# Optimization experiments

Measured on AMD Instinct MI355X. Metric: run time of the kernel, lower is better.

## Reference

```python
import jax, jax.numpy as jnp
import numpy as np

ADAPTERS = 40   # adapter_num, hard-coded by range(40) and tsv 40x40
CAPS = 3        # num_capsules
CLASS_DIM = 200 # MAX_SEQ
IN_CH = CAPS * CLASS_DIM  # 600
B = 256
D = 768
NUM_ITERS = 3


def squash(v, axis=-1):
    sq = jnp.sum(v * v, axis=axis, keepdims=True)
    return (sq / (1.0 + sq)) * v / jnp.sqrt(sq)


def setup_inputs() -> dict:
    key = jax.random.key(0)
    k0, k1, k2, k3, k4 = jax.random.split(key, 5)
    x = jax.random.normal(k0, (B, ADAPTERS, IN_CH), jnp.float32)
    s = jax.random.uniform(k1, (1,), jnp.float32) * 4.0 + 1.0  # gate temperature
    route_weights = jax.random.normal(k2, (ADAPTERS, CAPS, IN_CH, CLASS_DIM), jnp.float32)
    larger_w = jax.random.normal(k3, (D, CAPS), jnp.float32) * 0.1  # Linear(3,768) weight [out,in]
    larger_b = jnp.zeros((D,), jnp.float32)
    elarger = jax.random.normal(k4, (ADAPTERS, D), jnp.float32)     # Embedding(40,768)
    tsv = jnp.tril(jnp.ones((ADAPTERS, ADAPTERS), jnp.float32))
    return {"t": 20, "x": x, "s": s, "route_weights": route_weights,
            "larger_w": larger_w, "larger_b": larger_b, "elarger": elarger, "tsv": tsv}


def reference(t, x, s, route_weights, larger_w, larger_b, elarger, tsv):
    bz = x.shape[0]
    # per-adapter small matmuls, batched: priors[n,b,k,d] = sum_c x[b,k,c] * W[k,n,c,d]
    priors = jnp.einsum('bkc,kncd->nbkd', x, route_weights)[:, :, :, None, :]  # [3,B,40,1,200]
    tsv_t = tsv[t]                                   # [40]
    mask = jnp.where(tsv_t == 0, -10000.0, 0.0)      # [40]
    tsv_b = tsv_t[None, None, :, None, None]
    mask_b = mask[None, None, :, None, None]
    logits = jnp.zeros_like(priors)
    vote = None
    for i in range(NUM_ITERS):
        logits = logits * tsv_b + mask_b
        probs = jax.nn.softmax(logits, axis=2)       # my_softmax over adapter dim
        vote = jnp.sum(probs * priors, axis=2, keepdims=True)   # [3,B,1,1,200]
        out = squash(vote, axis=-1)
        if i != NUM_ITERS - 1:
            logits = logits + jnp.sum(priors * out, axis=-1, keepdims=True)
    # torch's .view(bz, length, -1) on a [3,B,1,1,200] tensor: row-major reinterpretation
    h = vote.reshape(bz, CLASS_DIM, CAPS)            # [B,200,3]
    h = h @ larger_w.T + larger_b                    # [B,200,768]
    g = jax.nn.sigmoid(s * elarger[t])               # [768] (broadcast of [1]*[768])
    return h * g
```

## Files before the change

kernel.cpp:

```cpp
#include <hip/hip_runtime.h>
#include <hip/hip_bf16.h>

#define ADAPTERS 40
#define CAPS 3
#define IN_CH 600
#define BSZ 256
#define DCLS 200
#define DMODEL 768

typedef __attribute__((ext_vector_type(8))) short short8;
typedef __attribute__((ext_vector_type(4))) float f32x4;
typedef __attribute__((ext_vector_type(4))) float f4v;

__global__ void k0_gw(const float* __restrict__ s_p,
                      const float* __restrict__ lw,
                      const float* __restrict__ lb,
                      const float* __restrict__ el,
                      const int* __restrict__ t_p,
                      float4* __restrict__ gw4) {
    int j = blockIdx.x * blockDim.x + threadIdx.x;
    if (j >= DMODEL) return;
    float s = s_p[0];
    int t = t_p[0];
    float e = el[t * DMODEL + j];
    float g = 1.0f / (1.0f + expf(-s * e));
    gw4[j] = make_float4(g * lw[j * 3 + 0], g * lw[j * 3 + 1],
                         g * lw[j * 3 + 2], g * lb[j]);
}

#define RP 40
#define NCHUNK 19

__device__ __forceinline__ void split2(float f0, float f1,
                                       unsigned& hi, unsigned& lo) {
    unsigned u0 = __float_as_uint(f0), u1 = __float_as_uint(f1);
    unsigned h0 = u0 & 0xFFFF0000u, h1 = u1 & 0xFFFF0000u;
    hi = (u0 >> 16) | h1;
    float l0 = f0 - __uint_as_float(h0);
    float l1 = f1 - __uint_as_float(h1);
    lo = (__float_as_uint(l0) >> 16) | (__float_as_uint(l1) & 0xFFFF0000u);
}

__global__ __launch_bounds__(256) void k1_priors(
    const float* __restrict__ x,
    const float* __restrict__ rw,
    const float* __restrict__ tsv,
    const int* __restrict__ t_p,
    float* __restrict__ priors)
{
    int kk = blockIdx.z;
    int t = t_p[0];
    if (tsv[t * ADAPTERS + kk] == 0.0f) return;

    int b0 = blockIdx.x * 128;
    int j0 = blockIdx.y * 128;

    __shared__ __align__(16) unsigned short Ahi[128 * RP];
    __shared__ __align__(16) unsigned short Alo[128 * RP];
    __shared__ __align__(16) unsigned short Bhi[128 * RP];
    __shared__ __align__(16) unsigned short Blo[128 * RP];

    int tid = threadIdx.x;
    int lane = tid & 63, w = tid >> 6;
    int lm = lane & 15, lq = lane >> 4;
    int m0w = (w & 1) * 64, n0w = (w >> 1) * 64;

    int a_bi = tid >> 1;
    int a_ci0 = (tid & 1) * 16;
    const float* a_row = x + ((size_t)(b0 + a_bi) * ADAPTERS + kk) * IN_CH;
    int b_jj = tid >> 1;
    int b_ci0 = (tid & 1) * 16;
    int j = j0 + b_jj;
    bool jvalid = (j < CAPS * DCLS);
    int cap = (j >= 2 * DCLS) ? 2 : ((j >= DCLS) ? 1 : 0);
    int d = j - cap * DCLS;
    const float* b_base = rw + ((size_t)(kk * 3 + cap) * IN_CH) * DCLS + d;

    f32x4 acc[4][4];
    #pragma unroll
    for (int mt = 0; mt < 4; mt++)
        #pragma unroll
        for (int nt = 0; nt < 4; nt++)
            acc[mt][nt] = (f32x4){0.f, 0.f, 0.f, 0.f};

    float4 ax[4];
    float  bx[16];

    {
        int c0 = 0;
        #pragma unroll
        for (int q = 0; q < 4; q++) {
            int c = c0 + a_ci0 + q * 4;
            ax[q] = (c + 4 <= IN_CH) ? *(const float4*)(a_row + c)
                                     : make_float4(0.f, 0.f, 0.f, 0.f);
        }
        #pragma unroll
        for (int i = 0; i < 16; i++) {
            int c = c0 + b_ci0 + i;
            bx[i] = (jvalid && c < IN_CH) ? b_base[(size_t)c * DCLS] : 0.f;
        }
    }

    for (int ch = 0; ch < NCHUNK; ch++) {
        unsigned ahi[8], alo[8], bhi[8], blo[8];
        #pragma unroll
        for (int q = 0; q < 4; q++) {
            split2(ax[q].x, ax[q].y, ahi[q * 2], alo[q * 2]);
            split2(ax[q].z, ax[q].w, ahi[q * 2 + 1], alo[q * 2 + 1]);
        }
        #pragma unroll
        for (int p = 0; p < 8; p++)
            split2(bx[2 * p], bx[2 * p + 1], bhi[p], blo[p]);

        __syncthreads();
        {
            unsigned* pa = (unsigned*)&Ahi[a_bi * RP + a_ci0];
            *(uint4*)pa = make_uint4(ahi[0], ahi[1], ahi[2], ahi[3]);
            *(uint4*)(pa + 4) = make_uint4(ahi[4], ahi[5], ahi[6], ahi[7]);
            unsigned* pl = (unsigned*)&Alo[a_bi * RP + a_ci0];
            *(uint4*)pl = make_uint4(alo[0], alo[1], alo[2], alo[3]);
            *(uint4*)(pl + 4) = make_uint4(alo[4], alo[5], alo[6], alo[7]);
            unsigned* pb = (unsigned*)&Bhi[b_jj * RP + b_ci0];
            *(uint4*)pb = make_uint4(bhi[0], bhi[1], bhi[2], bhi[3]);
            *(uint4*)(pb + 4) = make_uint4(bhi[4], bhi[5], bhi[6], bhi[7]);
            unsigned* pc = (unsigned*)&Blo[b_jj * RP + b_ci0];
            *(uint4*)pc = make_uint4(blo[0], blo[1], blo[2], blo[3]);
            *(uint4*)(pc + 4) = make_uint4(blo[4], blo[5], blo[6], blo[7]);
        }
        __syncthreads();

        if (ch + 1 < NCHUNK) {
            int c0 = (ch + 1) * 32;
            #pragma unroll
            for (int q = 0; q < 4; q++) {
                int c = c0 + a_ci0 + q * 4;
                ax[q] = (c + 4 <= IN_CH) ? *(const float4*)(a_row + c)
                                         : make_float4(0.f, 0.f, 0.f, 0.f);
            }
            #pragma unroll
            for (int i = 0; i < 16; i++) {
                int c = c0 + b_ci0 + i;
                bx[i] = (jvalid && c < IN_CH) ? b_base[(size_t)c * DCLS] : 0.f;
            }
        }

        short8 Afh[4], Afl[4];
        #pragma unroll
        for (int mt = 0; mt < 4; mt++) {
            int row = m0w + mt * 16 + lm;
            Afh[mt] = *(const short8*)&Ahi[row * RP + lq * 8];
            Afl[mt] = *(const short8*)&Alo[row * RP + lq * 8];
        }
        #pragma unroll
        for (int nt = 0; nt < 4; nt++) {
            int row = n0w + nt * 16 + lm;
            short8 bh = *(const short8*)&Bhi[row * RP + lq * 8];
            short8 bl = *(const short8*)&Blo[row * RP + lq * 8];
            #pragma unroll
            for (int mt = 0; mt < 4; mt++) {
                acc[mt][nt] = __builtin_amdgcn_mfma_f32_16x16x32_bf16(
                    bh, Afh[mt], acc[mt][nt], 0, 0, 0);
                acc[mt][nt] = __builtin_amdgcn_mfma_f32_16x16x32_bf16(
                    bl, Afh[mt], acc[mt][nt], 0, 0, 0);
                acc[mt][nt] = __builtin_amdgcn_mfma_f32_16x16x32_bf16(
                    bh, Afl[mt], acc[mt][nt], 0, 0, 0);
            }
        }
    }

    #pragma unroll
    for (int nt = 0; nt < 4; nt++) {
        int jc = j0 + n0w + nt * 16 + lq * 4;
        if (jc >= CAPS * DCLS) continue;
        int capc = (jc >= 2 * DCLS) ? 2 : ((jc >= DCLS) ? 1 : 0);
        int dc = jc - capc * DCLS;
        #pragma unroll
        for (int mt = 0; mt < 4; mt++) {
            int b = b0 + m0w + mt * 16 + lm;
            float* dst = priors +
                ((size_t)(capc * BSZ + b) * ADAPTERS + kk) * DCLS + dc;
            *(f4v*)dst = *(f4v*)&acc[mt][nt];
        }
    }
}

__global__ __launch_bounds__(256) void k2_route(
    const float* __restrict__ priors,
    const float* __restrict__ tsv,
    const int* __restrict__ t_p,
    float* __restrict__ vote)
{
    int nb = blockIdx.x;
    int n = nb >> 8, b = nb & 255;
    int tid = threadIdx.x;
    int lane = tid & 63, wid = tid >> 6;

    __shared__ float Ps[ADAPTERS * DCLS];
    __shared__ float vout[DCLS];
    __shared__ float act[ADAPTERS];
    __shared__ float a_s[ADAPTERS];
    __shared__ float probs_s[ADAPTERS];
    __shared__ int   klist[ADAPTERS];
    __shared__ int   nact_s;
    __shared__ float red[4];
    __shared__ float scl;

    int t = t_p[0];
    if (tid < ADAPTERS) {
        act[tid] = tsv[t * ADAPTERS + tid];
        a_s[tid] = 0.0f;
    }
    __syncthreads();

    if (tid == 0) {
        int c = 0;
        for (int k = 0; k < ADAPTERS; k++)
            if (act[k] != 0.0f) klist[c++] = k;
        nact_s = c;
    }

    {
        const float4* pb4 = (const float4*)
            (priors + (size_t)(n * BSZ + b) * ADAPTERS * DCLS);
        float4* Ps4 = (float4*)Ps;
        for (int i4 = tid; i4 < ADAPTERS * (DCLS / 4); i4 += 256) {
            int k = i4 / (DCLS / 4);
            if (act[k] != 0.0f) Ps4[i4] = pb4[i4];
        }
    }
    __syncthreads();

    int nact = nact_s;
    float cnt = (float)nact;

    int td = tid;
    float v = 0.0f;
    if (td < DCLS) {
        for (int ki = 0; ki < nact; ki++)
            v += Ps[klist[ki] * DCLS + td];
        v /= cnt;
    }

    for (int it = 0; it < 3; it++) {
        if (it > 0) {
            if (wid == 0) {
                bool on = (lane < ADAPTERS) && (act[lane] != 0.f);
                float val = on ? a_s[lane] : -3.0e38f;
                float m = val;
                for (int off = 32; off; off >>= 1)
                    m = fmaxf(m, __shfl_down(m, off));
                m = __shfl(m, 0);
                float e = on ? expf(val - m) : 0.f;
                float ssum = e;
                for (int off = 32; off; off >>= 1)
                    ssum += __shfl_down(ssum, off);
                ssum = __shfl(ssum, 0);
                if (lane < ADAPTERS) probs_s[lane] = e / ssum;
            }
            __syncthreads();
            v = 0.0f;
            if (td < DCLS) {
                for (int ki = 0; ki < nact; ki++) {
                    int k = klist[ki];
                    v += probs_s[k] * Ps[k * DCLS + td];
                }
            }
        }
        if (it == 2) break;

        float vv = (td < DCLS) ? v * v : 0.f;
        for (int off = 32; off; off >>= 1) vv += __shfl_down(vv, off);
        if (lane == 0) red[wid] = vv;
        __syncthreads();
        if (tid == 0) {
            float sq = red[0] + red[1] + red[2] + red[3];
            scl = sqrtf(sq) / (1.0f + sq);
        }
        __syncthreads();
        if (td < DCLS) vout[td] = v * scl;
        __syncthreads();

        for (int ki = wid; ki < nact; ki += 4) {
            int k = klist[ki];
            const float* row = Ps + k * DCLS;
            float p = row[lane] * vout[lane]
                    + row[lane + 64] * vout[lane + 64]
                    + row[lane + 128] * vout[lane + 128];
            if (lane < DCLS - 192) p += row[lane + 192] * vout[lane + 192];
            for (int off = 32; off; off >>= 1) p += __shfl_down(p, off);
            if (lane == 0) a_s[k] += p;
        }
        __syncthreads();
    }

    if (td < DCLS) vote[(size_t)n * BSZ * DCLS + b * DCLS + td] = v;
}

__global__ __launch_bounds__(256) void k3_out(
    const float* __restrict__ vote,
    const float4* __restrict__ gw4,
    float* __restrict__ out)
{
    __shared__ float vs[192];
    int tid = threadIdx.x;
    int r0 = blockIdx.x * 64;
    if (tid < 192) vs[tid] = vote[r0 * 3 + tid];
    __syncthreads();

    int lane = tid & 63;
    int ty = tid >> 6;
    int j = blockIdx.y * 256 + lane * 4;

    float4 g0 = gw4[j + 0];
    float4 g1 = gw4[j + 1];
    float4 g2 = gw4[j + 2];
    float4 g3 = gw4[j + 3];

    #pragma unroll
    for (int it = 0; it < 16; it++) {
        int rl = it * 4 + ty;
        float h0 = vs[rl * 3 + 0];
        float h1 = vs[rl * 3 + 1];
        float h2 = vs[rl * 3 + 2];
        f4v o;
        o.x = h0 * g0.x + h1 * g0.y + h2 * g0.z + g0.w;
        o.y = h0 * g1.x + h1 * g1.y + h2 * g1.z + g1.w;
        o.z = h0 * g2.x + h1 * g2.y + h2 * g2.z + g2.w;
        o.w = h0 * g3.x + h1 * g3.y + h2 * g3.z + g3.w;
        __builtin_nontemporal_store(o, (f4v*)(out + (size_t)(r0 + rl) * DMODEL + j));
    }
}

extern "C" void kernel_launch(void* const* d_in, const int* in_sizes, int n_in,
                              void* d_out, int out_size, void* d_ws, size_t ws_size,
                              hipStream_t stream) {
    const int*   t   = (const int*)d_in[0];
    const float* x   = (const float*)d_in[1];
    const float* s   = (const float*)d_in[2];
    const float* rw  = (const float*)d_in[3];
    const float* lw  = (const float*)d_in[4];
    const float* lb  = (const float*)d_in[5];
    const float* el  = (const float*)d_in[6];
    const float* tsv = (const float*)d_in[7];
    float* out = (float*)d_out;

    char* wsb = (char*)d_ws;
    float*  priors = (float*)wsb;
    float*  vote   = (float*)(wsb + 24576000);
    float4* gw4    = (float4*)(wsb + 25190400);

    k0_gw<<<dim3(3), dim3(256), 0, stream>>>(s, lw, lb, el, t, gw4);
    k1_priors<<<dim3(2, 5, ADAPTERS), dim3(256), 0, stream>>>(x, rw, tsv, t, priors);
    k2_route<<<dim3(CAPS * BSZ), dim3(256), 0, stream>>>(priors, tsv, t, vote);
    k3_out<<<dim3(BSZ * DCLS / 64, 3), dim3(256), 0, stream>>>(vote, gw4, out);
}
```

Measured before the change: 292.4 us.

## Use 512-thread blocks in priors GEMM and fuse gate computation into output kernel

After: 282.6 us. -3.4%, faster.

```diff
diff --git a/kernel.cpp b/kernel.cpp
--- a/kernel.cpp
+++ b/kernel.cpp
@@ -11,22 +11,6 @@
 typedef __attribute__((ext_vector_type(8))) short short8;
 typedef __attribute__((ext_vector_type(4))) float f32x4;
 typedef __attribute__((ext_vector_type(4))) float f4v;
-
-__global__ void k0_gw(const float* __restrict__ s_p,
-                      const float* __restrict__ lw,
-                      const float* __restrict__ lb,
-                      const float* __restrict__ el,
-                      const int* __restrict__ t_p,
-                      float4* __restrict__ gw4) {
-    int j = blockIdx.x * blockDim.x + threadIdx.x;
-    if (j >= DMODEL) return;
-    float s = s_p[0];
-    int t = t_p[0];
-    float e = el[t * DMODEL + j];
-    float g = 1.0f / (1.0f + expf(-s * e));
-    gw4[j] = make_float4(g * lw[j * 3 + 0], g * lw[j * 3 + 1],
-                         g * lw[j * 3 + 2], g * lb[j]);
-}
 
 #define RP 40
 #define NCHUNK 19
@@ -41,7 +25,7 @@
     lo = (__float_as_uint(l0) >> 16) | (__float_as_uint(l1) & 0xFFFF0000u);
 }
 
-__global__ __launch_bounds__(256) void k1_priors(
+__global__ __launch_bounds__(512) void k1_priors(
     const float* __restrict__ x,
     const float* __restrict__ rw,
     const float* __restrict__ tsv,
@@ -63,82 +47,78 @@
     int tid = threadIdx.x;
     int lane = tid & 63, w = tid >> 6;
     int lm = lane & 15, lq = lane >> 4;
-    int m0w = (w & 1) * 64, n0w = (w >> 1) * 64;
-
-    int a_bi = tid >> 1;
-    int a_ci0 = (tid & 1) * 16;
+    int m0w = (w & 1) * 64;
+    int n0w = (w >> 1) * 32;
+
+    int a_bi = tid >> 2;
+    int a_ci0 = (tid & 3) * 8;
     const float* a_row = x + ((size_t)(b0 + a_bi) * ADAPTERS + kk) * IN_CH;
-    int b_jj = tid >> 1;
-    int b_ci0 = (tid & 1) * 16;
+    int b_jj = tid >> 2;
+    int b_ci0 = (tid & 3) * 8;
     int j = j0 + b_jj;
     bool jvalid = (j < CAPS * DCLS);
     int cap = (j >= 2 * DCLS) ? 2 : ((j >= DCLS) ? 1 : 0);
     int d = j - cap * DCLS;
     const float* b_base = rw + ((size_t)(kk * 3 + cap) * IN_CH) * DCLS + d;
 
-    f32x4 acc[4][4];
+    f32x4 acc[4][2];
     #pragma unroll
     for (int mt = 0; mt < 4; mt++)
         #pragma unroll
-        for (int nt = 0; nt < 4; nt++)
+        for (int nt = 0; nt < 2; nt++)
             acc[mt][nt] = (f32x4){0.f, 0.f, 0.f, 0.f};
 
-    float4 ax[4];
-    float  bx[16];
+    float4 ax[2];
+    float  bx[8];
 
     {
         int c0 = 0;
         #pragma unroll
-        for (int q = 0; q < 4; q++) {
+        for (int q = 0; q < 2; q++) {
             int c = c0 + a_ci0 + q * 4;
             ax[q] = (c + 4 <= IN_CH) ? *(const float4*)(a_row + c)
                                      : make_float4(0.f, 0.f, 0.f, 0.f);
         }
         #pragma unroll
-        for (int i = 0; i < 16; i++) {
+        for (int i = 0; i < 8; i++) {
             int c = c0 + b_ci0 + i;
             bx[i] = (jvalid && c < IN_CH) ? b_base[(size_t)c * DCLS] : 0.f;
         }
     }
 
     for (int ch = 0; ch < NCHUNK; ch++) {
-        unsigned ahi[8], alo[8], bhi[8], blo[8];
-        #pragma unroll
-        for (int q = 0; q < 4; q++) {
-            split2(ax[q].x, ax[q].y, ahi[q * 2], alo[q * 2]);
-            split2(ax[q].z, ax[q].w, ahi[q * 2 + 1], alo[q * 2 + 1]);
-        }
-        #pragma unroll
-        for (int p = 0; p < 8; p++)
+        unsigned ahi[4], alo[4], bhi[4], blo[4];
+        split2(ax[0].x, ax[0].y, ahi[0], alo[0]);
+        split2(ax[0].z, ax[0].w, ahi[1], alo[1]);
+        split2(ax[1].x, ax[1].y, ahi[2], alo[2]);
+        split2(ax[1].z, ax[1].w, ahi[3], alo[3]);
+        #pragma unroll
+        for (int p = 0; p < 4; p++)
             split2(bx[2 * p], bx[2 * p + 1], bhi[p], blo[p]);
 
         __syncthreads();
         {
-            unsigned* pa = (unsigned*)&Ahi[a_bi * RP + a_ci0];
-            *(uint4*)pa = make_uint4(ahi[0], ahi[1], ahi[2], ahi[3]);
-            *(uint4*)(pa + 4) = make_uint4(ahi[4], ahi[5], ahi[6], ahi[7]);
-            unsigned* pl = (unsigned*)&Alo[a_bi * RP + a_ci0];
-            *(uint4*)pl = make_uint4(alo[0], alo[1], alo[2], alo[3]);
-            *(uint4*)(pl + 4) = make_uint4(alo[4], alo[5], alo[6], alo[7]);
-            unsigned* pb = (unsigned*)&Bhi[b_jj * RP + b_ci0];
-            *(uint4*)pb = make_uint4(bhi[0], bhi[1], bhi[2], bhi[3]);
-            *(uint4*)(pb + 4) = make_uint4(bhi[4], bhi[5], bhi[6], bhi[7]);
-            unsigned* pc = (unsigned*)&Blo[b_jj * RP + b_ci0];
-            *(uint4*)pc = make_uint4(blo[0], blo[1], blo[2], blo[3]);
-            *(uint4*)(pc + 4) = make_uint4(blo[4], blo[5], blo[6], blo[7]);
+            *(uint4*)((unsigned*)&Ahi[a_bi * RP + a_ci0]) =
+                make_uint4(ahi[0], ahi[1], ahi[2], ahi[3]);
+            *(uint4*)((unsigned*)&Alo[a_bi * RP + a_ci0]) =
+                make_uint4(alo[0], alo[1], alo[2], alo[3]);
+            *(uint4*)((unsigned*)&Bhi[b_jj * RP + b_ci0]) =
+                make_uint4(bhi[0], bhi[1], bhi[2], bhi[3]);
+            *(uint4*)((unsigned*)&Blo[b_jj * RP + b_ci0]) =
+                make_uint4(blo[0], blo[1], blo[2], blo[3]);
         }
         __syncthreads();
 
         if (ch + 1 < NCHUNK) {
             int c0 = (ch + 1) * 32;
             #pragma unroll
-            for (int q = 0; q < 4; q++) {
+            for (int q = 0; q < 2; q++) {
                 int c = c0 + a_ci0 + q * 4;
                 ax[q] = (c + 4 <= IN_CH) ? *(const float4*)(a_row + c)
                                          : make_float4(0.f, 0.f, 0.f, 0.f);
             }
             #pragma unroll
-            for (int i = 0; i < 16; i++) {
+            for (int i = 0; i < 8; i++) {
                 int c = c0 + b_ci0 + i;
                 bx[i] = (jvalid && c < IN_CH) ? b_base[(size_t)c * DCLS] : 0.f;
             }
@@ -152,7 +132,7 @@
             Afl[mt] = *(const short8*)&Alo[row * RP + lq * 8];
         }
         #pragma unroll
-        for (int nt = 0; nt < 4; nt++) {
+        for (int nt = 0; nt < 2; nt++) {
             int row = n0w + nt * 16 + lm;
             short8 bh = *(const short8*)&Bhi[row * RP + lq * 8];
             short8 bl = *(const short8*)&Blo[row * RP + lq * 8];
@@ -169,7 +149,7 @@
     }
 
     #pragma unroll
-    for (int nt = 0; nt < 4; nt++) {
+    for (int nt = 0; nt < 2; nt++) {
         int jc = j0 + n0w + nt * 16 + lq * 4;
         if (jc >= CAPS * DCLS) continue;
         int capc = (jc >= 2 * DCLS) ? 2 : ((jc >= DCLS) ? 1 : 0);
@@ -298,23 +278,38 @@
 
 __global__ __launch_bounds__(256) void k3_out(
     const float* __restrict__ vote,
-    const float4* __restrict__ gw4,
+    const float* __restrict__ s_p,
+    const float* __restrict__ lw,
+    const float* __restrict__ lb,
+    const float* __restrict__ el,
+    const int* __restrict__ t_p,
     float* __restrict__ out)
 {
     __shared__ float vs[192];
     int tid = threadIdx.x;
     int r0 = blockIdx.x * 64;
     if (tid < 192) vs[tid] = vote[r0 * 3 + tid];
-    __syncthreads();
 
     int lane = tid & 63;
     int ty = tid >> 6;
     int j = blockIdx.y * 256 + lane * 4;
 
-    float4 g0 = gw4[j + 0];
-    float4 g1 = gw4[j + 1];
-    float4 g2 = gw4[j + 2];
-    float4 g3 = gw4[j + 3];
+    int t = t_p[0];
+    float s = s_p[0];
+    float4 e4  = *(const float4*)(el + (size_t)t * DMODEL + j);
+    float4 lb4 = *(const float4*)(lb + j);
+    const float4* lw4 = (const float4*)(lw + (size_t)j * 3);
+    float4 w0 = lw4[0], w1 = lw4[1], w2 = lw4[2];
+    float ga = 1.0f / (1.0f + expf(-s * e4.x));
+    float gb = 1.0f / (1.0f + expf(-s * e4.y));
+    float gc = 1.0f / (1.0f + expf(-s * e4.z));
+    float gd = 1.0f / (1.0f + expf(-s * e4.w));
+    float4 g0 = make_float4(ga * w0.x, ga * w0.y, ga * w0.z, ga * lb4.x);
+    float4 g1 = make_float4(gb * w0.w, gb * w1.x, gb * w1.y, gb * lb4.y);
+    float4 g2 = make_float4(gc * w1.z, gc * w1.w, gc * w2.x, gc * lb4.z);
+    float4 g3 = make_float4(gd * w2.y, gd * w2.z, gd * w2.w, gd * lb4.w);
+
+    __syncthreads();
 
     #pragma unroll
     for (int it = 0; it < 16; it++) {
@@ -345,12 +340,10 @@
     float* out = (float*)d_out;
 
     char* wsb = (char*)d_ws;
-    float*  priors = (float*)wsb;
-    float*  vote   = (float*)(wsb + 24576000);
-    float4* gw4    = (float4*)(wsb + 25190400);
-
-    k0_gw<<<dim3(3), dim3(256), 0, stream>>>(s, lw, lb, el, t, gw4);
-    k1_priors<<<dim3(2, 5, ADAPTERS), dim3(256), 0, stream>>>(x, rw, tsv, t, priors);
+    float* priors = (float*)wsb;
+    float* vote   = (float*)(wsb + 24576000);
+
+    k1_priors<<<dim3(2, 5, ADAPTERS), dim3(512), 0, stream>>>(x, rw, tsv, t, priors);
     k2_route<<<dim3(CAPS * BSZ), dim3(256), 0, stream>>>(priors, tsv, t, vote);
-    k3_out<<<dim3(BSZ * DCLS / 64, 3), dim3(256), 0, stream>>>(vote, gw4, out);
-}
+    k3_out<<<dim3(BSZ * DCLS / 64, 3), dim3(256), 0, stream>>>(vote, s, lw, lb, el, t, out);
+}
```
